# Performance work log

Measured on AMD Instinct MI355X. Metric: run time of the kernel, lower is better.

Reference implementation:

```python
import jax, jax.numpy as jnp
import numpy as np

B, S, E, H = 1, 8192, 1024, 16
D = E // H
SEG_LENS = [2048, 4096, 8192]
DILATIONS = [1, 2, 4]


def setup_inputs() -> dict:
    key = jax.random.key(0)
    k0, k1, k2 = jax.random.split(key, 3)
    sc_in = 1.0 / np.sqrt(E)
    return {
        "x": jax.random.normal(k0, (B, S, E), jnp.float32),
        "w_qkv": jax.random.normal(k1, (3 * E, E), jnp.float32) * sc_in,
        "b_qkv": jnp.zeros((3 * E,), jnp.float32),
        "w_out": jax.random.normal(k2, (E, E), jnp.float32) * sc_in,
        "b_out": jnp.zeros((E,), jnp.float32),
    }


def _sdpa(q, k, v):
    # q,k,v: [B,H,N,D]; standard scaled dot-product attention (non-causal)
    scale = 1.0 / np.sqrt(q.shape[-1])
    scores = jnp.einsum('bhqd,bhkd->bhqk', q, k) * scale
    probs = jax.nn.softmax(scores, axis=-1)
    return jnp.einsum('bhqk,bhkd->bhqd', probs, v)


def reference(x, w_qkv, b_qkv, w_out, b_out):
    # QKV projection: torch Linear is x @ W^T + b
    qkv = x @ w_qkv.T + b_qkv                       # [B,S,3E]
    qkv = qkv.reshape(B, S, 3, H, D).transpose(2, 0, 3, 1, 4)  # [3,B,H,S,D]
    q, k, v = qkv[0], qkv[1], qkv[2]

    seg_outputs = []
    for seg_len, dil in zip(SEG_LENS, DILATIONS):
        if seg_len > S:
            continue
        if dil > 1:
            n = min(seg_len, S // dil)
            pos = np.arange(0, n * dil, dil)        # strided dilated gather
        else:
            pos = np.arange(seg_len)                # leading segment
        o = _sdpa(q[:, :, pos], k[:, :, pos], v[:, :, pos])
        # scatter back to full length (zero elsewhere); also handles zero-padding
        full = jnp.zeros((B, H, S, D), x.dtype).at[:, :, pos, :].set(o)
        seg_outputs.append(full)

    if len(seg_outputs) == 0:
        out = jnp.zeros((B, H, S, D), x.dtype)
    else:
        out = seg_outputs[0]
        for so in seg_outputs[1:]:
            out = out + so
        out = out / len(seg_outputs)                # stack(...).mean(0)

    out = out.transpose(0, 2, 1, 3).reshape(B, S, E)
    return out @ w_out.T + b_out
```

## Files before the change

### kernel.cpp

```cpp
#include <hip/hip_runtime.h>


typedef __attribute__((ext_vector_type(8))) short bf16x8;
typedef __attribute__((ext_vector_type(4))) float f32x4;

#define MFMA(a, b, c) __builtin_amdgcn_mfma_f32_16x16x32_bf16((a), (b), (c), 0, 0, 0)

static __device__ __forceinline__ unsigned short f2bf(float f) {
  unsigned int u = __float_as_uint(f);
  unsigned int r = (u + 0x7FFFu + ((u >> 16) & 1u)) >> 16;
  return (unsigned short)r;
}

static __device__ __forceinline__ int perm64(int n) {
  return (n & ~63) | (((n & 15) << 2) | ((n >> 4) & 3));
}

__global__ void cvt_f32_bf16(const float* __restrict__ in,
                             unsigned short* __restrict__ out, int n8) {
  int i = blockIdx.x * blockDim.x + threadIdx.x;
  if (i >= n8) return;
  const float4* p = (const float4*)in + (size_t)i * 2;
  float4 a = p[0];
  float4 b = p[1];
  union { bf16x8 v; unsigned short u[8]; } o;
  o.u[0] = f2bf(a.x); o.u[1] = f2bf(a.y); o.u[2] = f2bf(a.z); o.u[3] = f2bf(a.w);
  o.u[4] = f2bf(b.x); o.u[5] = f2bf(b.y); o.u[6] = f2bf(b.z); o.u[7] = f2bf(b.w);
  *((bf16x8*)out + i) = o.v;
}

template <int EPILOGUE>
__global__ __launch_bounds__(256, 2) void gemm_bt(
    const unsigned short* __restrict__ A, const unsigned short* __restrict__ B,
    const float* __restrict__ bias, void* __restrict__ Cout,
    unsigned short* __restrict__ vt1, unsigned short* __restrict__ vt2,
    unsigned short* __restrict__ vt3, int N, int K) {
  __shared__ unsigned short At[128 * 32];
  __shared__ unsigned short Bt[128 * 32];
  const int tid = threadIdx.x;
  const int wave = tid >> 6, lane = tid & 63;
  const int quad = lane >> 4, lc = lane & 15;
  const int wm = (wave >> 1) * 64, wn = (wave & 1) * 64;
  const int m0 = blockIdx.x * 128, n0 = blockIdx.y * 128;

  f32x4 acc[4][4] = {};

  for (int k0 = 0; k0 < K; k0 += 32) {
    __syncthreads();
#pragma unroll
    for (int issue = 0; issue < 2; ++issue) {
      const int cbase = issue * 256 + wave * 64;
      const int c = cbase + lane;
      const int row = c >> 2, col8 = (c & 3) * 8;
      __builtin_amdgcn_global_load_lds(
          (const __attribute__((address_space(1))) void*)&A[(size_t)(m0 + row) * K + k0 + col8],
          (__attribute__((address_space(3))) void*)&At[cbase * 8], 16, 0, 0);
      __builtin_amdgcn_global_load_lds(
          (const __attribute__((address_space(1))) void*)&B[(size_t)(n0 + row) * K + k0 + col8],
          (__attribute__((address_space(3))) void*)&Bt[cbase * 8], 16, 0, 0);
    }
    __syncthreads();
    bf16x8 af[4], bfr[4];
#pragma unroll
    for (int t = 0; t < 4; ++t)
      af[t] = *(const bf16x8*)&At[(wm + t * 16 + lc) * 32 + quad * 8];
#pragma unroll
    for (int t = 0; t < 4; ++t)
      bfr[t] = *(const bf16x8*)&Bt[(wn + t * 16 + lc) * 32 + quad * 8];
#pragma unroll
    for (int i = 0; i < 4; ++i)
#pragma unroll
      for (int j = 0; j < 4; ++j)
        acc[i][j] = MFMA(af[i], bfr[j], acc[i][j]);
  }

#pragma unroll
  for (int i = 0; i < 4; ++i) {
#pragma unroll
    for (int j = 0; j < 4; ++j) {
      const int gcol = n0 + wn + j * 16 + lc;
      const float bs = bias[gcol];
#pragma unroll
      for (int r = 0; r < 4; ++r) {
        const int grow = m0 + wm + i * 16 + quad * 4 + r;
        const float v = acc[i][j][r] + bs;
        if (EPILOGUE == 0) {
          const int which = gcol >> 10, rem = gcol & 1023;
          const int hh = rem >> 6, d = rem & 63;
          unsigned short* qkv = (unsigned short*)Cout;
          if (which == 0) {
            qkv[((size_t)hh * 8192 + grow) * 64 + d] = f2bf(v * 0.125f);
          } else if (which == 1) {
            qkv[((size_t)(16 + hh) * 8192 + grow) * 64 + d] = f2bf(v);
          } else {
            const unsigned short b = f2bf(v);
            const int s = grow;
            if (s < 2048)
              vt1[((size_t)hh * 64 + d) * 2048 + perm64(s)] = b;
            if ((s & 1) == 0)
              vt2[((size_t)hh * 64 + d) * 4096 + perm64(s >> 1)] = b;
            if ((s & 3) == 0)
              vt3[((size_t)hh * 64 + d) * 2048 + perm64(s >> 2)] = b;
          }
        } else {
          ((float*)Cout)[(size_t)grow * N + gcol] = v;
        }
      }
    }
  }
}

__global__ __launch_bounds__(256, 2) void flash_seg(
    const unsigned short* __restrict__ qkvb, const unsigned short* __restrict__ vt,
    float* __restrict__ attn, int Nk, int dil) {
  __shared__ unsigned short Kt[64 * 72];
  __shared__ unsigned short Vt[80 * 72];
  __shared__ unsigned short Pt[4][16 * 72];

  const int tid = threadIdx.x;
  const int wave = tid >> 6, lane = tid & 63;
  const int quad = lane >> 4, lc = lane & 15;
  const int h = blockIdx.y;
  const int qt = blockIdx.x;

  const unsigned short* qh = qkvb + (size_t)h * 8192 * 64;
  const unsigned short* kh = qkvb + (size_t)(16 + h) * 8192 * 64;
  const unsigned short* vh = vt + (size_t)h * 64 * Nk;

  {
    const int r = 64 + (tid >> 4), c4 = (tid & 15) * 4;
    const unsigned long long ones = 0x3F803F803F803F80ull;
    *(unsigned long long*)&Vt[r * 72 + c4] = (r == 64) ? ones : 0ull;
  }

  const int qrow = qt * 64 + wave * 16 + lc;
  const bf16x8 qf0 = *(const bf16x8*)&qh[(size_t)qrow * dil * 64 + quad * 8];
  const bf16x8 qf1 = *(const bf16x8*)&qh[(size_t)qrow * dil * 64 + quad * 8 + 32];

  __syncthreads();
  const bf16x8 vone0 = *(const bf16x8*)&Vt[(64 + lc) * 72 + quad * 8];
  const bf16x8 vone1 = *(const bf16x8*)&Vt[(64 + lc) * 72 + quad * 8 + 32];

  f32x4 oacc[4] = {};
  f32x4 lacc = {};

  const int srow = tid >> 3, scol8 = (tid & 7) * 8;

  bf16x8 kg0 = *(const bf16x8*)&kh[(size_t)srow * dil * 64 + scol8];
  bf16x8 kg1 = *(const bf16x8*)&kh[(size_t)(srow + 32) * dil * 64 + scol8];
  bf16x8 vg0 = *(const bf16x8*)&vh[(size_t)srow * Nk + scol8];
  bf16x8 vg1 = *(const bf16x8*)&vh[(size_t)(srow + 32) * Nk + scol8];

  for (int kb = 0; kb < Nk; kb += 64) {
    __syncthreads();
    *(bf16x8*)&Kt[srow * 72 + scol8] = kg0;
    *(bf16x8*)&Kt[(srow + 32) * 72 + scol8] = kg1;
    *(bf16x8*)&Vt[srow * 72 + scol8] = vg0;
    *(bf16x8*)&Vt[(srow + 32) * 72 + scol8] = vg1;
    __syncthreads();

    if (kb + 64 < Nk) {
      const int nk = kb + 64;
      kg0 = *(const bf16x8*)&kh[(size_t)(nk + srow) * dil * 64 + scol8];
      kg1 = *(const bf16x8*)&kh[(size_t)(nk + srow + 32) * dil * 64 + scol8];
      vg0 = *(const bf16x8*)&vh[(size_t)srow * Nk + nk + scol8];
      vg1 = *(const bf16x8*)&vh[(size_t)(srow + 32) * Nk + nk + scol8];
    }

    f32x4 sacc[4] = {};
#pragma unroll
    for (int jb = 0; jb < 4; ++jb) {
      bf16x8 b0 = *(const bf16x8*)&Kt[(jb * 16 + lc) * 72 + quad * 8];
      bf16x8 b1 = *(const bf16x8*)&Kt[(jb * 16 + lc) * 72 + quad * 8 + 32];
      sacc[jb] = MFMA(qf0, b0, sacc[jb]);
      sacc[jb] = MFMA(qf1, b1, sacc[jb]);
    }

#pragma unroll
    for (int jb = 0; jb < 4; ++jb)
#pragma unroll
      for (int r = 0; r < 4; ++r) sacc[jb][r] = __expf(sacc[jb][r]);

#pragma unroll
    for (int r = 0; r < 4; ++r) {
      const unsigned int a0 = __float_as_uint(sacc[0][r]) + 0x8000u;
      const unsigned int a1 = __float_as_uint(sacc[1][r]) + 0x8000u;
      const unsigned int a2 = __float_as_uint(sacc[2][r]) + 0x8000u;
      const unsigned int a3 = __float_as_uint(sacc[3][r]) + 0x8000u;
      uint2 w;
      w.x = __builtin_amdgcn_perm(a1, a0, 0x07060302u);
      w.y = __builtin_amdgcn_perm(a3, a2, 0x07060302u);
      *(uint2*)&Pt[wave][(quad * 4 + r) * 72 + lc * 4] = w;
    }

    const bf16x8 pf0 = *(const bf16x8*)&Pt[wave][lc * 72 + quad * 8];
    const bf16x8 pf1 = *(const bf16x8*)&Pt[wave][lc * 72 + quad * 8 + 32];

#pragma unroll
    for (int nb = 0; nb < 4; ++nb) {
      bf16x8 v0 = *(const bf16x8*)&Vt[(nb * 16 + lc) * 72 + quad * 8];
      bf16x8 v1 = *(const bf16x8*)&Vt[(nb * 16 + lc) * 72 + quad * 8 + 32];
      oacc[nb] = MFMA(pf0, v0, oacc[nb]);
      oacc[nb] = MFMA(pf1, v1, oacc[nb]);
    }
    lacc = MFMA(pf0, vone0, lacc);
    lacc = MFMA(pf1, vone1, lacc);
  }

#pragma unroll
  for (int r = 0; r < 4; ++r) {
    const float l = __shfl(lacc[r], lane & 48, 64);
    const float inv = 1.0f / (3.0f * l);
    const int row = wave * 16 + quad * 4 + r;
    const size_t s = (size_t)(qt * 64 + row) * dil;
#pragma unroll
    for (int nb = 0; nb < 4; ++nb) {
      const int d = nb * 16 + lc;
      atomicAdd(&attn[s * 1024 + (size_t)h * 64 + d], oacc[nb][r] * inv);
    }
  }
}

extern "C" void kernel_launch(void* const* d_in, const int* in_sizes, int n_in,
                              void* d_out, int out_size, void* d_ws, size_t ws_size,
                              hipStream_t stream) {
  const float* x     = (const float*)d_in[0];
  const float* w_qkv = (const float*)d_in[1];
  const float* b_qkv = (const float*)d_in[2];
  const float* w_out = (const float*)d_in[3];
  const float* b_out = (const float*)d_in[4];
  float* out = (float*)d_out;

  char* ws = (char*)d_ws;
  unsigned short* qkvb  = (unsigned short*)(ws);
  unsigned short* vt1   = (unsigned short*)(ws + 33554432);
  unsigned short* vt2   = (unsigned short*)(ws + 37748736);
  unsigned short* vt3   = (unsigned short*)(ws + 46137344);
  float*          attn  = (float*)(ws + 50331648);
  unsigned short* wqkvb = (unsigned short*)(ws + 83886080);
  unsigned short* woutb = (unsigned short*)(ws + 90177536);
  unsigned short* xb    = (unsigned short*)(ws + 92274688);
  unsigned short* a3b   = xb;

  hipMemsetAsync(attn, 0, (size_t)8192 * 1024 * 4, stream);

  cvt_f32_bf16<<<dim3(8388608 / 8 / 256), dim3(256), 0, stream>>>(x, xb, 8388608 / 8);
  cvt_f32_bf16<<<dim3(3145728 / 8 / 256), dim3(256), 0, stream>>>(w_qkv, wqkvb, 3145728 / 8);
  cvt_f32_bf16<<<dim3(1048576 / 8 / 256), dim3(256), 0, stream>>>(w_out, woutb, 1048576 / 8);

  gemm_bt<0><<<dim3(64, 24), dim3(256), 0, stream>>>(xb, wqkvb, b_qkv, qkvb,
                                                     vt1, vt2, vt3, 3072, 1024);

  flash_seg<<<dim3(32, 16), dim3(256), 0, stream>>>(qkvb, vt1, attn, 2048, 1);
  flash_seg<<<dim3(64, 16), dim3(256), 0, stream>>>(qkvb, vt2, attn, 4096, 2);
  flash_seg<<<dim3(32, 16), dim3(256), 0, stream>>>(qkvb, vt3, attn, 2048, 4);

  cvt_f32_bf16<<<dim3(8388608 / 8 / 256), dim3(256), 0, stream>>>(attn, a3b, 8388608 / 8);

  gemm_bt<1><<<dim3(64, 8), dim3(256), 0, stream>>>(a3b, woutb, b_out, out,
                                                    nullptr, nullptr, nullptr, 1024, 1024);
}
```

Before: 417.5 us.

## Merge segment attention launches, drop atomics, add V transpose and combine kernels

Replaces the three flash_seg launches with one flash_all launch over a z dimension. Each block now covers 128 query rows with two m-blocks per wave, so each K/V tile loaded to LDS is reused across twice as many rows. exp is switched to exp2, with log2(e) folded into the Q scale. The scattered per-element V transpose stores in the QKV GEMM epilogue move into a separate LDS-tiled transpose kernel. Atomic accumulation into a memset buffer is replaced by plain stores into three per-segment buffers, summed by a combine kernel that also converts to bf16. This adds two launches and extra fp32 intermediate traffic.

```diff
diff --git a/kernel.cpp b/kernel.cpp
--- a/kernel.cpp
+++ b/kernel.cpp
@@ -5,15 +5,17 @@
 typedef __attribute__((ext_vector_type(4))) float f32x4;
 
 #define MFMA(a, b, c) __builtin_amdgcn_mfma_f32_16x16x32_bf16((a), (b), (c), 0, 0, 0)
+
+#if __has_builtin(__builtin_amdgcn_exp2f)
+#define EXP2(x) __builtin_amdgcn_exp2f(x)
+#else
+#define EXP2(x) exp2f(x)
+#endif
 
 static __device__ __forceinline__ unsigned short f2bf(float f) {
   unsigned int u = __float_as_uint(f);
   unsigned int r = (u + 0x7FFFu + ((u >> 16) & 1u)) >> 16;
   return (unsigned short)r;
-}
-
-static __device__ __forceinline__ int perm64(int n) {
-  return (n & ~63) | (((n & 15) << 2) | ((n >> 4) & 3));
 }
 
 __global__ void cvt_f32_bf16(const float* __restrict__ in,
@@ -32,9 +34,7 @@
 template <int EPILOGUE>
 __global__ __launch_bounds__(256, 2) void gemm_bt(
     const unsigned short* __restrict__ A, const unsigned short* __restrict__ B,
-    const float* __restrict__ bias, void* __restrict__ Cout,
-    unsigned short* __restrict__ vt1, unsigned short* __restrict__ vt2,
-    unsigned short* __restrict__ vt3, int N, int K) {
+    const float* __restrict__ bias, void* __restrict__ Cout, int N, int K) {
   __shared__ unsigned short At[128 * 32];
   __shared__ unsigned short Bt[128 * 32];
   const int tid = threadIdx.x;
@@ -87,21 +87,8 @@
         if (EPILOGUE == 0) {
           const int which = gcol >> 10, rem = gcol & 1023;
           const int hh = rem >> 6, d = rem & 63;
-          unsigned short* qkv = (unsigned short*)Cout;
-          if (which == 0) {
-            qkv[((size_t)hh * 8192 + grow) * 64 + d] = f2bf(v * 0.125f);
-          } else if (which == 1) {
-            qkv[((size_t)(16 + hh) * 8192 + grow) * 64 + d] = f2bf(v);
-          } else {
-            const unsigned short b = f2bf(v);
-            const int s = grow;
-            if (s < 2048)
-              vt1[((size_t)hh * 64 + d) * 2048 + perm64(s)] = b;
-            if ((s & 1) == 0)
-              vt2[((size_t)hh * 64 + d) * 4096 + perm64(s >> 1)] = b;
-            if ((s & 3) == 0)
-              vt3[((size_t)hh * 64 + d) * 2048 + perm64(s >> 2)] = b;
-          }
+          const float vs = (which == 0) ? v * 0.18033688f : v;
+          ((unsigned short*)Cout)[(((size_t)(which * 16 + hh)) * 8192 + grow) * 64 + d] = f2bf(vs);
         } else {
           ((float*)Cout)[(size_t)grow * N + gcol] = v;
         }
@@ -110,18 +97,63 @@
   }
 }
 
-__global__ __launch_bounds__(256, 2) void flash_seg(
-    const unsigned short* __restrict__ qkvb, const unsigned short* __restrict__ vt,
-    float* __restrict__ attn, int Nk, int dil) {
+__global__ void transpose_v(const unsigned short* __restrict__ v,
+                            unsigned short* __restrict__ vt1,
+                            unsigned short* __restrict__ vt2,
+                            unsigned short* __restrict__ vt3) {
+  __shared__ unsigned short Tt[64 * 72];
+  const int tid = threadIdx.x;
+  const int h = blockIdx.y;
+  const int bx = blockIdx.x;
+  const unsigned short* src = v + (size_t)h * 8192 * 64;
+  unsigned short* dst;
+  int dil, Nk, t0;
+  if (bx < 32)      { dst = vt1; dil = 1; Nk = 2048; t0 = bx; }
+  else if (bx < 96) { dst = vt2; dil = 2; Nk = 4096; t0 = bx - 32; }
+  else              { dst = vt3; dil = 4; Nk = 2048; t0 = bx - 96; }
+  dst += (size_t)h * 64 * Nk;
+  const int j0 = t0 * 64;
+#pragma unroll
+  for (int it = 0; it < 2; ++it) {
+    const int slot = tid + it * 256;
+    const int jj = slot >> 3, c8 = (slot & 7) * 8;
+    *(bf16x8*)&Tt[jj * 72 + c8] =
+        *(const bf16x8*)&src[(size_t)(j0 + jj) * dil * 64 + c8];
+  }
+  __syncthreads();
+  const int d = tid >> 2, pg = (tid & 3) * 16;
+  union { bf16x8 v2[2]; unsigned short u[16]; } ob;
+#pragma unroll
+  for (int t = 0; t < 16; ++t) {
+    const int pos = pg + t;
+    const int jj = (pos & 3) * 16 + (pos >> 2);
+    ob.u[t] = Tt[jj * 72 + d];
+  }
+  *(bf16x8*)&dst[(size_t)d * Nk + j0 + pg] = ob.v2[0];
+  *(bf16x8*)&dst[(size_t)d * Nk + j0 + pg + 8] = ob.v2[1];
+}
+
+__global__ __launch_bounds__(256, 2) void flash_all(
+    const unsigned short* __restrict__ qkvb,
+    const unsigned short* __restrict__ vt1, float* __restrict__ o1,
+    const unsigned short* __restrict__ vt2, float* __restrict__ o2,
+    const unsigned short* __restrict__ vt3, float* __restrict__ o3) {
   __shared__ unsigned short Kt[64 * 72];
   __shared__ unsigned short Vt[80 * 72];
-  __shared__ unsigned short Pt[4][16 * 72];
+  __shared__ unsigned short Pt[4][32 * 72];
+
+  const int z = blockIdx.z;
+  const int Nk = (z == 1) ? 4096 : 2048;
+  const int qt = blockIdx.x;
+  if (qt * 128 >= Nk) return;
+  const int dil = 1 << z;
+  const unsigned short* vt = (z == 0) ? vt1 : (z == 1) ? vt2 : vt3;
+  float* o = (z == 0) ? o1 : (z == 1) ? o2 : o3;
 
   const int tid = threadIdx.x;
   const int wave = tid >> 6, lane = tid & 63;
   const int quad = lane >> 4, lc = lane & 15;
   const int h = blockIdx.y;
-  const int qt = blockIdx.x;
 
   const unsigned short* qh = qkvb + (size_t)h * 8192 * 64;
   const unsigned short* kh = qkvb + (size_t)(16 + h) * 8192 * 64;
@@ -129,20 +161,23 @@
 
   {
     const int r = 64 + (tid >> 4), c4 = (tid & 15) * 4;
-    const unsigned long long ones = 0x3F803F803F803F80ull;
-    *(unsigned long long*)&Vt[r * 72 + c4] = (r == 64) ? ones : 0ull;
-  }
-
-  const int qrow = qt * 64 + wave * 16 + lc;
-  const bf16x8 qf0 = *(const bf16x8*)&qh[(size_t)qrow * dil * 64 + quad * 8];
-  const bf16x8 qf1 = *(const bf16x8*)&qh[(size_t)qrow * dil * 64 + quad * 8 + 32];
+    *(unsigned long long*)&Vt[r * 72 + c4] = 0x3F803F803F803F80ull;
+  }
+
+  bf16x8 qf[2][2];
+#pragma unroll
+  for (int mb = 0; mb < 2; ++mb) {
+    const int qrow = qt * 128 + wave * 32 + mb * 16 + lc;
+    qf[mb][0] = *(const bf16x8*)&qh[(size_t)qrow * dil * 64 + quad * 8];
+    qf[mb][1] = *(const bf16x8*)&qh[(size_t)qrow * dil * 64 + quad * 8 + 32];
+  }
 
   __syncthreads();
   const bf16x8 vone0 = *(const bf16x8*)&Vt[(64 + lc) * 72 + quad * 8];
   const bf16x8 vone1 = *(const bf16x8*)&Vt[(64 + lc) * 72 + quad * 8 + 32];
 
-  f32x4 oacc[4] = {};
-  f32x4 lacc = {};
+  f32x4 oacc[2][4] = {};
+  f32x4 lacc[2] = {};
 
   const int srow = tid >> 3, scol8 = (tid & 7) * 8;
 
@@ -167,58 +202,100 @@
       vg1 = *(const bf16x8*)&vh[(size_t)(srow + 32) * Nk + nk + scol8];
     }
 
-    f32x4 sacc[4] = {};
+    f32x4 sacc[2][4] = {};
 #pragma unroll
     for (int jb = 0; jb < 4; ++jb) {
-      bf16x8 b0 = *(const bf16x8*)&Kt[(jb * 16 + lc) * 72 + quad * 8];
-      bf16x8 b1 = *(const bf16x8*)&Kt[(jb * 16 + lc) * 72 + quad * 8 + 32];
-      sacc[jb] = MFMA(qf0, b0, sacc[jb]);
-      sacc[jb] = MFMA(qf1, b1, sacc[jb]);
-    }
-
-#pragma unroll
-    for (int jb = 0; jb < 4; ++jb)
-#pragma unroll
-      for (int r = 0; r < 4; ++r) sacc[jb][r] = __expf(sacc[jb][r]);
-
+      const bf16x8 b0 = *(const bf16x8*)&Kt[(jb * 16 + lc) * 72 + quad * 8];
+      const bf16x8 b1 = *(const bf16x8*)&Kt[(jb * 16 + lc) * 72 + quad * 8 + 32];
+#pragma unroll
+      for (int mb = 0; mb < 2; ++mb) {
+        sacc[mb][jb] = MFMA(qf[mb][0], b0, sacc[mb][jb]);
+        sacc[mb][jb] = MFMA(qf[mb][1], b1, sacc[mb][jb]);
+      }
+    }
+
+#pragma unroll
+    for (int mb = 0; mb < 2; ++mb)
+#pragma unroll
+      for (int jb = 0; jb < 4; ++jb)
+#pragma unroll
+        for (int r = 0; r < 4; ++r) sacc[mb][jb][r] = EXP2(sacc[mb][jb][r]);
+
+#pragma unroll
+    for (int mb = 0; mb < 2; ++mb)
+#pragma unroll
+      for (int r = 0; r < 4; ++r) {
+        const unsigned int a0 = __float_as_uint(sacc[mb][0][r]) + 0x8000u;
+        const unsigned int a1 = __float_as_uint(sacc[mb][1][r]) + 0x8000u;
+        const unsigned int a2 = __float_as_uint(sacc[mb][2][r]) + 0x8000u;
+        const unsigned int a3 = __float_as_uint(sacc[mb][3][r]) + 0x8000u;
+        uint2 w;
+        w.x = __builtin_amdgcn_perm(a1, a0, 0x07060302u);
+        w.y = __builtin_amdgcn_perm(a3, a2, 0x07060302u);
+        *(uint2*)&Pt[wave][(mb * 16 + quad * 4 + r) * 72 + lc * 4] = w;
+      }
+
+    bf16x8 pf[2][2];
+#pragma unroll
+    for (int mb = 0; mb < 2; ++mb) {
+      pf[mb][0] = *(const bf16x8*)&Pt[wave][(mb * 16 + lc) * 72 + quad * 8];
+      pf[mb][1] = *(const bf16x8*)&Pt[wave][(mb * 16 + lc) * 72 + quad * 8 + 32];
+    }
+#pragma unroll
+    for (int nb = 0; nb < 4; ++nb) {
+      const bf16x8 v0 = *(const bf16x8*)&Vt[(nb * 16 + lc) * 72 + quad * 8];
+      const bf16x8 v1 = *(const bf16x8*)&Vt[(nb * 16 + lc) * 72 + quad * 8 + 32];
+#pragma unroll
+      for (int mb = 0; mb < 2; ++mb) {
+        oacc[mb][nb] = MFMA(pf[mb][0], v0, oacc[mb][nb]);
+        oacc[mb][nb] = MFMA(pf[mb][1], v1, oacc[mb][nb]);
+      }
+    }
+#pragma unroll
+    for (int mb = 0; mb < 2; ++mb) {
+      lacc[mb] = MFMA(pf[mb][0], vone0, lacc[mb]);
+      lacc[mb] = MFMA(pf[mb][1], vone1, lacc[mb]);
+    }
+  }
+
+#pragma unroll
+  for (int mb = 0; mb < 2; ++mb)
 #pragma unroll
     for (int r = 0; r < 4; ++r) {
-      const unsigned int a0 = __float_as_uint(sacc[0][r]) + 0x8000u;
-      const unsigned int a1 = __float_as_uint(sacc[1][r]) + 0x8000u;
-      const unsigned int a2 = __float_as_uint(sacc[2][r]) + 0x8000u;
-      const unsigned int a3 = __float_as_uint(sacc[3][r]) + 0x8000u;
-      uint2 w;
-      w.x = __builtin_amdgcn_perm(a1, a0, 0x07060302u);
-      w.y = __builtin_amdgcn_perm(a3, a2, 0x07060302u);
-      *(uint2*)&Pt[wave][(quad * 4 + r) * 72 + lc * 4] = w;
-    }
-
-    const bf16x8 pf0 = *(const bf16x8*)&Pt[wave][lc * 72 + quad * 8];
-    const bf16x8 pf1 = *(const bf16x8*)&Pt[wave][lc * 72 + quad * 8 + 32];
-
-#pragma unroll
-    for (int nb = 0; nb < 4; ++nb) {
-      bf16x8 v0 = *(const bf16x8*)&Vt[(nb * 16 + lc) * 72 + quad * 8];
-      bf16x8 v1 = *(const bf16x8*)&Vt[(nb * 16 + lc) * 72 + quad * 8 + 32];
-      oacc[nb] = MFMA(pf0, v0, oacc[nb]);
-      oacc[nb] = MFMA(pf1, v1, oacc[nb]);
-    }
-    lacc = MFMA(pf0, vone0, lacc);
-    lacc = MFMA(pf1, vone1, lacc);
-  }
-
-#pragma unroll
-  for (int r = 0; r < 4; ++r) {
-    const float l = __shfl(lacc[r], lane & 48, 64);
-    const float inv = 1.0f / (3.0f * l);
-    const int row = wave * 16 + quad * 4 + r;
-    const size_t s = (size_t)(qt * 64 + row) * dil;
-#pragma unroll
-    for (int nb = 0; nb < 4; ++nb) {
-      const int d = nb * 16 + lc;
-      atomicAdd(&attn[s * 1024 + (size_t)h * 64 + d], oacc[nb][r] * inv);
-    }
-  }
+      const int row = wave * 32 + mb * 16 + quad * 4 + r;
+      const float inv = 1.0f / (3.0f * lacc[mb][r]);
+      const size_t base = (size_t)(qt * 128 + row) * 1024 + h * 64;
+#pragma unroll
+      for (int nb = 0; nb < 4; ++nb)
+        o[base + nb * 16 + lc] = oacc[mb][nb][r] * inv;
+    }
+}
+
+__global__ void combine(const float* __restrict__ o1, const float* __restrict__ o2,
+                        const float* __restrict__ o3,
+                        unsigned short* __restrict__ a3b) {
+  const int idx = blockIdx.x * 256 + threadIdx.x;
+  const int s = idx >> 7, e = (idx & 127) * 8;
+  float acc[8] = {};
+  if (s < 2048) {
+    const float4* p = (const float4*)&o1[(size_t)s * 1024 + e];
+#pragma unroll
+    for (int t = 0; t < 4; ++t) { acc[t] += ((const float*)p)[t]; acc[4 + t] += ((const float*)p)[4 + t]; }
+  }
+  if (!(s & 1)) {
+    const float4* p = (const float4*)&o2[(size_t)(s >> 1) * 1024 + e];
+#pragma unroll
+    for (int t = 0; t < 4; ++t) { acc[t] += ((const float*)p)[t]; acc[4 + t] += ((const float*)p)[4 + t]; }
+  }
+  if (!(s & 3)) {
+    const float4* p = (const float4*)&o3[(size_t)(s >> 2) * 1024 + e];
+#pragma unroll
+    for (int t = 0; t < 4; ++t) { acc[t] += ((const float*)p)[t]; acc[4 + t] += ((const float*)p)[4 + t]; }
+  }
+  union { bf16x8 v; unsigned short u[8]; } ob;
+#pragma unroll
+  for (int t = 0; t < 8; ++t) ob.u[t] = f2bf(acc[t]);
+  *(bf16x8*)&a3b[(size_t)s * 1024 + e] = ob.v;
 }
 
 extern "C" void kernel_launch(void* const* d_in, const int* in_sizes, int n_in,
@@ -233,30 +310,29 @@
 
   char* ws = (char*)d_ws;
   unsigned short* qkvb  = (unsigned short*)(ws);
-  unsigned short* vt1   = (unsigned short*)(ws + 33554432);
-  unsigned short* vt2   = (unsigned short*)(ws + 37748736);
-  unsigned short* vt3   = (unsigned short*)(ws + 46137344);
-  float*          attn  = (float*)(ws + 50331648);
+  float*          o1    = (float*)(ws + 33554432);
+  float*          o3    = (float*)(ws + 41943040);
+  unsigned short* vt1   = (unsigned short*)(ws + 50331648);
+  unsigned short* vt2   = (unsigned short*)(ws + 54525952);
+  unsigned short* vt3   = (unsigned short*)(ws + 62914560);
+  float*          o2    = (float*)(ws + 67108864);
   unsigned short* wqkvb = (unsigned short*)(ws + 83886080);
   unsigned short* woutb = (unsigned short*)(ws + 90177536);
   unsigned short* xb    = (unsigned short*)(ws + 92274688);
   unsigned short* a3b   = xb;
 
-  hipMemsetAsync(attn, 0, (size_t)8192 * 1024 * 4, stream);
-
   cvt_f32_bf16<<<dim3(8388608 / 8 / 256), dim3(256), 0, stream>>>(x, xb, 8388608 / 8);
   cvt_f32_bf16<<<dim3(3145728 / 8 / 256), dim3(256), 0, stream>>>(w_qkv, wqkvb, 3145728 / 8);
   cvt_f32_bf16<<<dim3(1048576 / 8 / 256), dim3(256), 0, stream>>>(w_out, woutb, 1048576 / 8);
 
-  gemm_bt<0><<<dim3(64, 24), dim3(256), 0, stream>>>(xb, wqkvb, b_qkv, qkvb,
-                                                     vt1, vt2, vt3, 3072, 1024);
-
-  flash_seg<<<dim3(32, 16), dim3(256), 0, stream>>>(qkvb, vt1, attn, 2048, 1);
-  flash_seg<<<dim3(64, 16), dim3(256), 0, stream>>>(qkvb, vt2, attn, 4096, 2);
-  flash_seg<<<dim3(32, 16), dim3(256), 0, stream>>>(qkvb, vt3, attn, 2048, 4);
-
-  cvt_f32_bf16<<<dim3(8388608 / 8 / 256), dim3(256), 0, stream>>>(attn, a3b, 8388608 / 8);
-
-  gemm_bt<1><<<dim3(64, 8), dim3(256), 0, stream>>>(a3b, woutb, b_out, out,
-                                                    nullptr, nullptr, nullptr, 1024, 1024);
-}
+  gemm_bt<0><<<dim3(64, 24), dim3(256), 0, stream>>>(xb, wqkvb, b_qkv, qkvb, 3072, 1024);
+
+  transpose_v<<<dim3(128, 16), dim3(256), 0, stream>>>(qkvb + (size_t)32 * 8192 * 64,
+                                                       vt1, vt2, vt3);
+
+  flash_all<<<dim3(32, 16, 3), dim3(256), 0, stream>>>(qkvb, vt1, o1, vt2, o2, vt3, o3);
+
+  combine<<<dim3(4096), dim3(256), 0, stream>>>(o1, o2, o3, a3b);
+
+  gemm_bt<1><<<dim3(64, 8), dim3(256), 0, stream>>>(a3b, woutb, b_out, out, 1024, 1024);
+}
```

New measurement: 357.9 us. -14.3%, faster.
